# Performance work log

Measured on AMD Instinct MI355X. Metric: run time of the kernel, lower is better.

The kernel has to match this reference:

```python
import jax, jax.numpy as jnp
import numpy as np
from jax.scipy.special import ndtri

D = 1024
BITS = 4
K = 2 ** BITS
N = 4096


def _rotation_matrix(d, seed):
    # Haar-distributed random orthogonal matrix via QR with sign fix,
    # matching generate_rotation_matrix in the torch source.
    g = np.random.default_rng(seed).standard_normal((d, d)).astype(np.float32)
    Q, R = np.linalg.qr(g)
    s = np.sign(np.diag(R))
    s[s == 0] = 1.0
    return jnp.asarray((Q * s[None, :]).astype(np.float32))


def _lloyd_max_centroids(k):
    # Per-coordinate scalar codebook for a standard Gaussian (Lloyd-Max init
    # via inverse-CDF midpoints), analogous to LloydMaxCodebook.centroids [K].
    probs = (jnp.arange(k, dtype=jnp.float32) + 0.5) / k
    return ndtri(probs).astype(jnp.float32)


def setup_inputs() -> dict:
    key = jax.random.key(0)
    x = jax.random.normal(key, (N, D), dtype=jnp.float32)
    Pi = _rotation_matrix(D, seed=42)          # [d, d]
    centroids = _lloyd_max_centroids(K)        # [K]
    return {"x": x, "Pi": Pi, "centroids": centroids}


def reference(x, Pi, centroids):
    # rotate: y = x @ Pi^T
    y = x @ Pi.T                               # [N, d]
    # per-coordinate nearest-centroid argmin over K
    diffs = jnp.abs(y[..., None] - centroids)  # [N, d, K]
    indices = jnp.argmin(diffs, axis=-1)       # [N, d] int
    # dequantize: gather centroids, then unrotate x_hat = y_hat @ Pi
    y_hat = centroids[indices]                 # [N, d]
    x_hat = y_hat @ Pi                         # [N, d]
    return x_hat, indices
```

## Files before the change

### kernel.cpp

```cpp
#include <hip/hip_runtime.h>
#include <hip/hip_bf16.h>

#define TQ_D   1024
#define TQ_KC  16
#define MERGE_K 512
#define TQ_TOL  1.0e-4f
#define LCAP    1024

typedef __attribute__((ext_vector_type(8))) short bf16x8;
typedef __attribute__((ext_vector_type(4))) float f32x4;

__device__ __forceinline__ unsigned short f2bf(float f) {
    union { __hip_bfloat16 h; unsigned short s; } u;
    u.h = __float2bfloat16(f);
    return u.s;
}
__device__ __forceinline__ float bf2f(unsigned short s) {
    union { unsigned int u; float f; } v;
    v.u = (unsigned int)s << 16;
    return v.f;
}

__global__ __launch_bounds__(512)
void tq_rq_mfma(const float* __restrict__ X,
                const float* __restrict__ Pi,
                const float* __restrict__ Cent,
                float* __restrict__ OutIdx,
                unsigned* __restrict__ Counter,
                unsigned* __restrict__ List,
                unsigned cap)
{
    __shared__ unsigned short XhS[128][40];
    __shared__ unsigned short XlS[128][40];
    __shared__ unsigned short PhS[64][40];
    __shared__ unsigned short PlS[64][40];
    __shared__ unsigned lcount;
    __shared__ unsigned gbase;
    __shared__ unsigned llist[LCAP];

    const int tid  = threadIdx.x;
    const int lane = tid & 63;
    const int wv   = tid >> 6;
    const int m0 = blockIdx.y * 128;
    const int n0 = blockIdx.x * 64;
    const int wr = (wv >> 1) * 32;
    const int wc = (wv & 1) * 32;
    const int l15 = lane & 15;
    const int k8  = (lane >> 4) * 8;

    const int srow = tid >> 2;
    const int scol = (tid & 3) * 8;
    const int brow = tid >> 3;
    const int bcol = (tid & 7) * 4;

    const float* aP = X  + (size_t)(m0 + srow) * TQ_D + scol;
    const float* bP = Pi + (size_t)(n0 + brow) * TQ_D + bcol;

    if (tid == 0) lcount = 0;

    f32x4 acc[2][2];
#pragma unroll
    for (int i = 0; i < 2; ++i)
#pragma unroll
        for (int j = 0; j < 2; ++j)
#pragma unroll
            for (int r = 0; r < 4; ++r) acc[i][j][r] = 0.0f;

    float4 va[2], vb;
#pragma unroll
    for (int q = 0; q < 2; ++q) va[q] = *(const float4*)(aP + 4 * q);
    vb = *(const float4*)(bP);

#pragma unroll
    for (int q = 0; q < 2; ++q) {
        ushort4 ah, al;
        const float* fa = (const float*)&va[q];
        ah.x = f2bf(fa[0]); al.x = f2bf(fa[0] - bf2f(ah.x));
        ah.y = f2bf(fa[1]); al.y = f2bf(fa[1] - bf2f(ah.y));
        ah.z = f2bf(fa[2]); al.z = f2bf(fa[2] - bf2f(ah.z));
        ah.w = f2bf(fa[3]); al.w = f2bf(fa[3] - bf2f(ah.w));
        *(ushort4*)&XhS[srow][scol + 4 * q] = ah;
        *(ushort4*)&XlS[srow][scol + 4 * q] = al;
    }
    {
        ushort4 bh, bl;
        const float* fb = (const float*)&vb;
        bh.x = f2bf(fb[0]); bl.x = f2bf(fb[0] - bf2f(bh.x));
        bh.y = f2bf(fb[1]); bl.y = f2bf(fb[1] - bf2f(bh.y));
        bh.z = f2bf(fb[2]); bl.z = f2bf(fb[2] - bf2f(bh.z));
        bh.w = f2bf(fb[3]); bl.w = f2bf(fb[3] - bf2f(bh.w));
        *(ushort4*)&PhS[brow][bcol] = bh;
        *(ushort4*)&PlS[brow][bcol] = bl;
    }
    __syncthreads();

    for (int kt = 0; kt < 32; ++kt) {
        const bool more = (kt + 1) < 32;
        if (more) {
            const float* ap = aP + (kt + 1) * 32;
            const float* bp = bP + (kt + 1) * 32;
#pragma unroll
            for (int q = 0; q < 2; ++q) va[q] = *(const float4*)(ap + 4 * q);
            vb = *(const float4*)(bp);
        }

        bf16x8 afh[2], afl[2], bfh[2], bfl[2];
#pragma unroll
        for (int i = 0; i < 2; ++i) {
            afh[i] = *(const bf16x8*)&XhS[wr + i * 16 + l15][k8];
            afl[i] = *(const bf16x8*)&XlS[wr + i * 16 + l15][k8];
        }
#pragma unroll
        for (int j = 0; j < 2; ++j) {
            bfh[j] = *(const bf16x8*)&PhS[wc + j * 16 + l15][k8];
            bfl[j] = *(const bf16x8*)&PlS[wc + j * 16 + l15][k8];
        }

#pragma unroll
        for (int i = 0; i < 2; ++i)
#pragma unroll
            for (int j = 0; j < 2; ++j) {
                acc[i][j] = __builtin_amdgcn_mfma_f32_16x16x32_bf16(
                    afh[i], bfh[j], acc[i][j], 0, 0, 0);
                acc[i][j] = __builtin_amdgcn_mfma_f32_16x16x32_bf16(
                    afl[i], bfh[j], acc[i][j], 0, 0, 0);
                acc[i][j] = __builtin_amdgcn_mfma_f32_16x16x32_bf16(
                    afh[i], bfl[j], acc[i][j], 0, 0, 0);
                acc[i][j] = __builtin_amdgcn_mfma_f32_16x16x32_bf16(
                    afl[i], bfl[j], acc[i][j], 0, 0, 0);
            }

        if (more) {
            __syncthreads();
#pragma unroll
            for (int q = 0; q < 2; ++q) {
                ushort4 ah, al;
                const float* fa = (const float*)&va[q];
                ah.x = f2bf(fa[0]); al.x = f2bf(fa[0] - bf2f(ah.x));
                ah.y = f2bf(fa[1]); al.y = f2bf(fa[1] - bf2f(ah.y));
                ah.z = f2bf(fa[2]); al.z = f2bf(fa[2] - bf2f(ah.z));
                ah.w = f2bf(fa[3]); al.w = f2bf(fa[3] - bf2f(ah.w));
                *(ushort4*)&XhS[srow][scol + 4 * q] = ah;
                *(ushort4*)&XlS[srow][scol + 4 * q] = al;
            }
            {
                ushort4 bh, bl;
                const float* fb = (const float*)&vb;
                bh.x = f2bf(fb[0]); bl.x = f2bf(fb[0] - bf2f(bh.x));
                bh.y = f2bf(fb[1]); bl.y = f2bf(fb[1] - bf2f(bh.y));
                bh.z = f2bf(fb[2]); bl.z = f2bf(fb[2] - bf2f(bh.z));
                bh.w = f2bf(fb[3]); bl.w = f2bf(fb[3] - bf2f(bh.w));
                *(ushort4*)&PhS[brow][bcol] = bh;
                *(ushort4*)&PlS[brow][bcol] = bl;
            }
            __syncthreads();
        }
    }

    float c[TQ_KC];
#pragma unroll
    for (int q = 0; q < TQ_KC; ++q) c[q] = Cent[q];

#pragma unroll
    for (int i = 0; i < 2; ++i)
#pragma unroll
        for (int j = 0; j < 2; ++j)
#pragma unroll
            for (int r = 0; r < 4; ++r) {
                const int row = m0 + wr + i * 16 + (lane >> 4) * 4 + r;
                const int col = n0 + wc + j * 16 + l15;
                const float y = acc[i][j][r];
                int best = 0;
                float bd = fabsf(y - c[0]);
#pragma unroll
                for (int q = 1; q < TQ_KC; ++q) {
                    const float d = fabsf(y - c[q]);
                    if (d < bd) { bd = d; best = q; }
                }
                float dist = 1e30f;
#pragma unroll
                for (int q = 0; q < TQ_KC - 1; ++q) {
                    const float mid = 0.5f * (c[q] + c[q + 1]);
                    dist = fminf(dist, fabsf(y - mid));
                }
                if (dist < TQ_TOL) {
                    const unsigned id = ((unsigned)row << 10) | (unsigned)col;
                    const unsigned ls = atomicAdd(&lcount, 1u);
                    if (ls < LCAP) {
                        llist[ls] = id;
                    } else {
                        const unsigned gs = atomicAdd(Counter, 1u);
                        if (gs < cap) List[gs] = id;
                    }
                }
                OutIdx[(size_t)row * TQ_D + col] = (float)best;
            }

    __syncthreads();
    if (tid == 0) {
        const unsigned cnt = min(lcount, (unsigned)LCAP);
        gbase = (cnt > 0) ? atomicAdd(Counter, cnt) : 0u;
    }
    __syncthreads();
    const unsigned cnt = min(lcount, (unsigned)LCAP);
    for (unsigned s = tid; s < cnt; s += 512) {
        const unsigned g = gbase + s;
        if (g < cap) List[g] = llist[s];
    }
}

__global__ __launch_bounds__(256)
void tq_fixup_lds(const float* __restrict__ X,
                  const float* __restrict__ Pi,
                  const float* __restrict__ Cent,
                  float* __restrict__ OutIdx,
                  const unsigned* __restrict__ Counter,
                  const unsigned* __restrict__ List,
                  unsigned cap)
{
    __shared__ float Rows[8][2][1024];
    __shared__ float part[8][2];
    __shared__ unsigned ids[8];

    const int tid = threadIdx.x;
    const unsigned count = min(*Counter, cap);

    for (unsigned base = blockIdx.x * 8; base < count; base += gridDim.x * 8) {
        const unsigned nsus = min(8u, count - base);

        if (tid < 8) ids[tid] = (tid < nsus) ? List[base + tid] : 0u;
        __syncthreads();

#pragma unroll
        for (int q = 0; q < 16; ++q) {
            const int lin = q * 256 + tid;
            const int sus = lin >> 9;
            const int rowsel = (lin >> 8) & 1;
            const int f4 = lin & 255;
            if ((unsigned)sus < nsus) {
                const unsigned id = ids[sus];
                const int m = id >> 10;
                const int n = id & (TQ_D - 1);
                const float* src = rowsel ? (Pi + (size_t)n * TQ_D)
                                          : (X + (size_t)m * TQ_D);
                *(float4*)&Rows[sus][rowsel][f4 * 4] =
                    *(const float4*)(src + f4 * 4);
            }
        }
        __syncthreads();

        if (tid < 16 && (unsigned)(tid >> 1) < nsus) {
            const int sus = tid >> 1;
            const int p = tid & 1;
            const int kb = p * MERGE_K;
            float a = 0.0f;
            for (int k = 0; k < MERGE_K; k += 4) {
                const float4 xa = *(const float4*)&Rows[sus][0][kb + k];
                const float4 pa = *(const float4*)&Rows[sus][1][kb + k];
                a = fmaf(xa.x, pa.x, a);
                a = fmaf(xa.y, pa.y, a);
                a = fmaf(xa.z, pa.z, a);
                a = fmaf(xa.w, pa.w, a);
            }
            part[sus][p] = a;
        }
        __syncthreads();

        if (tid < (int)nsus) {
            const float y = part[tid][0] + part[tid][1];
            float c[TQ_KC];
#pragma unroll
            for (int q = 0; q < TQ_KC; ++q) c[q] = Cent[q];
            int best = 0;
            float bd = fabsf(y - c[0]);
#pragma unroll
            for (int q = 1; q < TQ_KC; ++q) {
                const float d = fabsf(y - c[q]);
                if (d < bd) { bd = d; best = q; }
            }
            const unsigned id = ids[tid];
            OutIdx[(size_t)(id >> 10) * TQ_D + (id & (TQ_D - 1))] = (float)best;
        }
        __syncthreads();
    }
}

__global__ __launch_bounds__(512)
void tq_dq_mfma(const float* __restrict__ IdxF,
                const float* __restrict__ Pi,
                const float* __restrict__ Cent,
                float* __restrict__ Xhat)
{
    __shared__ unsigned short Ys[128][40];
    __shared__ unsigned short Ps[64][40];
    __shared__ unsigned short csb[TQ_KC];

    const int tid  = threadIdx.x;
    const int lane = tid & 63;
    const int wv   = tid >> 6;
    const int m0 = blockIdx.y * 128;
    const int n0 = blockIdx.x * 64;
    const int wr = (wv >> 1) * 32;
    const int wc = (wv & 1) * 32;
    const int l15 = lane & 15;
    const int k8  = (lane >> 4) * 8;

    const int srow = tid >> 2;
    const int scol = (tid & 3) * 8;
    const int bk = tid >> 4;
    const int bnq = (tid & 15) * 4;

    const float* aP = IdxF + (size_t)(m0 + srow) * TQ_D + scol;
    const float* bP = Pi + (size_t)bk * TQ_D + n0 + bnq;

    if (tid < TQ_KC) csb[tid] = f2bf(Cent[tid]);

    f32x4 acc[2][2];
#pragma unroll
    for (int i = 0; i < 2; ++i)
#pragma unroll
        for (int j = 0; j < 2; ++j)
#pragma unroll
            for (int r = 0; r < 4; ++r) acc[i][j][r] = 0.0f;

    float4 va[2], vb;
#pragma unroll
    for (int q = 0; q < 2; ++q) va[q] = *(const float4*)(aP + 4 * q);
    vb = *(const float4*)(bP);

    __syncthreads();

#pragma unroll
    for (int q = 0; q < 2; ++q) {
        ushort4 w;
        const float* fa = (const float*)&va[q];
        w.x = csb[(int)fa[0] & 15];
        w.y = csb[(int)fa[1] & 15];
        w.z = csb[(int)fa[2] & 15];
        w.w = csb[(int)fa[3] & 15];
        *(ushort4*)&Ys[srow][scol + 4 * q] = w;
    }
    {
        const float* fb = (const float*)&vb;
        Ps[bnq + 0][bk] = f2bf(fb[0]);
        Ps[bnq + 1][bk] = f2bf(fb[1]);
        Ps[bnq + 2][bk] = f2bf(fb[2]);
        Ps[bnq + 3][bk] = f2bf(fb[3]);
    }
    __syncthreads();

    for (int kt = 0; kt < 32; ++kt) {
        const bool more = (kt + 1) < 32;
        if (more) {
            const float* ap = aP + (kt + 1) * 32;
            const float* bp = bP + (size_t)(kt + 1) * 32 * TQ_D;
#pragma unroll
            for (int q = 0; q < 2; ++q) va[q] = *(const float4*)(ap + 4 * q);
            vb = *(const float4*)(bp);
        }

        bf16x8 af[2], bfr[2];
#pragma unroll
        for (int i = 0; i < 2; ++i)
            af[i] = *(const bf16x8*)&Ys[wr + i * 16 + l15][k8];
#pragma unroll
        for (int j = 0; j < 2; ++j)
            bfr[j] = *(const bf16x8*)&Ps[wc + j * 16 + l15][k8];

#pragma unroll
        for (int i = 0; i < 2; ++i)
#pragma unroll
            for (int j = 0; j < 2; ++j)
                acc[i][j] = __builtin_amdgcn_mfma_f32_16x16x32_bf16(
                    af[i], bfr[j], acc[i][j], 0, 0, 0);

        if (more) {
            __syncthreads();
#pragma unroll
            for (int q = 0; q < 2; ++q) {
                ushort4 w;
                const float* fa = (const float*)&va[q];
                w.x = csb[(int)fa[0] & 15];
                w.y = csb[(int)fa[1] & 15];
                w.z = csb[(int)fa[2] & 15];
                w.w = csb[(int)fa[3] & 15];
                *(ushort4*)&Ys[srow][scol + 4 * q] = w;
            }
            {
                const float* fb = (const float*)&vb;
                Ps[bnq + 0][bk] = f2bf(fb[0]);
                Ps[bnq + 1][bk] = f2bf(fb[1]);
                Ps[bnq + 2][bk] = f2bf(fb[2]);
                Ps[bnq + 3][bk] = f2bf(fb[3]);
            }
            __syncthreads();
        }
    }

#pragma unroll
    for (int i = 0; i < 2; ++i)
#pragma unroll
        for (int j = 0; j < 2; ++j)
#pragma unroll
            for (int r = 0; r < 4; ++r) {
                const int row = wr + i * 16 + (lane >> 4) * 4 + r;
                const int col = wc + j * 16 + l15;
                Xhat[(size_t)(m0 + row) * TQ_D + n0 + col] = acc[i][j][r];
            }
}

extern "C" void kernel_launch(void* const* d_in, const int* in_sizes, int n_in,
                              void* d_out, int out_size, void* d_ws, size_t ws_size,
                              hipStream_t stream)
{
    const float* x    = (const float*)d_in[0];
    const float* Pi   = (const float*)d_in[1];
    const float* cent = (const float*)d_in[2];
    float* out = (float*)d_out;

    const int ND = in_sizes[0];
    const int N  = ND / TQ_D;

    float* xhat = out;
    float* oidx = out + ND;

    unsigned* counter = (unsigned*)xhat;
    unsigned* list    = (unsigned*)xhat + 16;
    const unsigned cap = (unsigned)(ND - 16);

    hipMemsetAsync(counter, 0, 4, stream);

    dim3 grid1(TQ_D / 64, N / 128);
    tq_rq_mfma<<<grid1, 512, 0, stream>>>(x, Pi, cent, oidx, counter, list, cap);

    tq_fixup_lds<<<1024, 256, 0, stream>>>(x, Pi, cent, oidx, counter, list, cap);

    tq_dq_mfma<<<grid1, 512, 0, stream>>>(oidx, Pi, cent, xhat);
}
```

Baseline: 107.4 us.

## Pre-split inputs into bf16 hi/lo buffers and dequantize from bf16 centroids

```diff
diff --git a/kernel.cpp b/kernel.cpp
--- a/kernel.cpp
+++ b/kernel.cpp
@@ -8,6 +8,7 @@
 #define LCAP    1024
 
 typedef __attribute__((ext_vector_type(8))) short bf16x8;
+typedef __attribute__((ext_vector_type(8))) unsigned short ushort8;
 typedef __attribute__((ext_vector_type(4))) float f32x4;
 
 __device__ __forceinline__ unsigned short f2bf(float f) {
@@ -19,6 +20,188 @@
     union { unsigned int u; float f; } v;
     v.u = (unsigned int)s << 16;
     return v.f;
+}
+
+__global__ __launch_bounds__(256)
+void tq_split(const float* __restrict__ In,
+              unsigned short* __restrict__ Hi,
+              unsigned short* __restrict__ Lo,
+              int total4)
+{
+    for (int i = blockIdx.x * 256 + threadIdx.x; i < total4;
+         i += gridDim.x * 256) {
+        const float4 v = *((const float4*)In + i);
+        ushort4 h, l;
+        h.x = f2bf(v.x); l.x = f2bf(v.x - bf2f(h.x));
+        h.y = f2bf(v.y); l.y = f2bf(v.y - bf2f(h.y));
+        h.z = f2bf(v.z); l.z = f2bf(v.z - bf2f(h.z));
+        h.w = f2bf(v.w); l.w = f2bf(v.w - bf2f(h.w));
+        *((ushort4*)Hi + i) = h;
+        *((ushort4*)Lo + i) = l;
+    }
+}
+
+__global__ __launch_bounds__(512)
+void tq_rq_mfma_pre(const unsigned short* __restrict__ Xh,
+                    const unsigned short* __restrict__ Xl,
+                    const unsigned short* __restrict__ Ph,
+                    const unsigned short* __restrict__ Pl,
+                    const float* __restrict__ Cent,
+                    float* __restrict__ OutIdx,
+                    unsigned short* __restrict__ Yh,
+                    unsigned* __restrict__ Counter,
+                    unsigned* __restrict__ List,
+                    unsigned cap)
+{
+    __shared__ unsigned short XhS[128][40];
+    __shared__ unsigned short XlS[128][40];
+    __shared__ unsigned short PhS[64][40];
+    __shared__ unsigned short PlS[64][40];
+    __shared__ unsigned lcount;
+    __shared__ unsigned gbase;
+    __shared__ unsigned llist[LCAP];
+
+    const int tid  = threadIdx.x;
+    const int lane = tid & 63;
+    const int wv   = tid >> 6;
+    const int m0 = blockIdx.y * 128;
+    const int n0 = blockIdx.x * 64;
+    const int wr = (wv >> 1) * 32;
+    const int wc = (wv & 1) * 32;
+    const int l15 = lane & 15;
+    const int k8  = (lane >> 4) * 8;
+
+    const int srow = tid >> 2;
+    const int scol = (tid & 3) * 8;
+    const int brow = tid >> 3;
+    const int bcol = (tid & 7) * 4;
+
+    const unsigned short* aH = Xh + (size_t)(m0 + srow) * TQ_D + scol;
+    const unsigned short* aL = Xl + (size_t)(m0 + srow) * TQ_D + scol;
+    const unsigned short* bH = Ph + (size_t)(n0 + brow) * TQ_D + bcol;
+    const unsigned short* bL = Pl + (size_t)(n0 + brow) * TQ_D + bcol;
+
+    if (tid == 0) lcount = 0;
+
+    f32x4 acc[2][2];
+#pragma unroll
+    for (int i = 0; i < 2; ++i)
+#pragma unroll
+        for (int j = 0; j < 2; ++j)
+#pragma unroll
+            for (int r = 0; r < 4; ++r) acc[i][j][r] = 0.0f;
+
+    ushort8 vah, val;
+    ushort4 vbh, vbl;
+    vah = *(const ushort8*)(aH);
+    val = *(const ushort8*)(aL);
+    vbh = *(const ushort4*)(bH);
+    vbl = *(const ushort4*)(bL);
+
+    *(ushort8*)&XhS[srow][scol] = vah;
+    *(ushort8*)&XlS[srow][scol] = val;
+    *(ushort4*)&PhS[brow][bcol] = vbh;
+    *(ushort4*)&PlS[brow][bcol] = vbl;
+    __syncthreads();
+
+    for (int kt = 0; kt < 32; ++kt) {
+        const bool more = (kt + 1) < 32;
+        if (more) {
+            const int off = (kt + 1) * 32;
+            vah = *(const ushort8*)(aH + off);
+            val = *(const ushort8*)(aL + off);
+            vbh = *(const ushort4*)(bH + off);
+            vbl = *(const ushort4*)(bL + off);
+        }
+
+        bf16x8 afh[2], afl[2], bfh[2], bfl[2];
+#pragma unroll
+        for (int i = 0; i < 2; ++i) {
+            afh[i] = *(const bf16x8*)&XhS[wr + i * 16 + l15][k8];
+            afl[i] = *(const bf16x8*)&XlS[wr + i * 16 + l15][k8];
+        }
+#pragma unroll
+        for (int j = 0; j < 2; ++j) {
+            bfh[j] = *(const bf16x8*)&PhS[wc + j * 16 + l15][k8];
+            bfl[j] = *(const bf16x8*)&PlS[wc + j * 16 + l15][k8];
+        }
+
+#pragma unroll
+        for (int i = 0; i < 2; ++i)
+#pragma unroll
+            for (int j = 0; j < 2; ++j) {
+                acc[i][j] = __builtin_amdgcn_mfma_f32_16x16x32_bf16(
+                    afh[i], bfh[j], acc[i][j], 0, 0, 0);
+                acc[i][j] = __builtin_amdgcn_mfma_f32_16x16x32_bf16(
+                    afl[i], bfh[j], acc[i][j], 0, 0, 0);
+                acc[i][j] = __builtin_amdgcn_mfma_f32_16x16x32_bf16(
+                    afh[i], bfl[j], acc[i][j], 0, 0, 0);
+                acc[i][j] = __builtin_amdgcn_mfma_f32_16x16x32_bf16(
+                    afl[i], bfl[j], acc[i][j], 0, 0, 0);
+            }
+
+        if (more) {
+            __syncthreads();
+            *(ushort8*)&XhS[srow][scol] = vah;
+            *(ushort8*)&XlS[srow][scol] = val;
+            *(ushort4*)&PhS[brow][bcol] = vbh;
+            *(ushort4*)&PlS[brow][bcol] = vbl;
+            __syncthreads();
+        }
+    }
+
+    float c[TQ_KC];
+#pragma unroll
+    for (int q = 0; q < TQ_KC; ++q) c[q] = Cent[q];
+
+#pragma unroll
+    for (int i = 0; i < 2; ++i)
+#pragma unroll
+        for (int j = 0; j < 2; ++j)
+#pragma unroll
+            for (int r = 0; r < 4; ++r) {
+                const int row = m0 + wr + i * 16 + (lane >> 4) * 4 + r;
+                const int col = n0 + wc + j * 16 + l15;
+                const float y = acc[i][j][r];
+                int best = 0;
+                float bd = fabsf(y - c[0]);
+#pragma unroll
+                for (int q = 1; q < TQ_KC; ++q) {
+                    const float d = fabsf(y - c[q]);
+                    if (d < bd) { bd = d; best = q; }
+                }
+                float dist = 1e30f;
+#pragma unroll
+                for (int q = 0; q < TQ_KC - 1; ++q) {
+                    const float mid = 0.5f * (c[q] + c[q + 1]);
+                    dist = fminf(dist, fabsf(y - mid));
+                }
+                if (dist < TQ_TOL) {
+                    const unsigned id = ((unsigned)row << 10) | (unsigned)col;
+                    const unsigned ls = atomicAdd(&lcount, 1u);
+                    if (ls < LCAP) {
+                        llist[ls] = id;
+                    } else {
+                        const unsigned gs = atomicAdd(Counter, 1u);
+                        if (gs < cap) List[gs] = id;
+                    }
+                }
+                const size_t e = (size_t)row * TQ_D + col;
+                OutIdx[e] = (float)best;
+                Yh[e] = f2bf(c[best]);
+            }
+
+    __syncthreads();
+    if (tid == 0) {
+        const unsigned cnt = min(lcount, (unsigned)LCAP);
+        gbase = (cnt > 0) ? atomicAdd(Counter, cnt) : 0u;
+    }
+    __syncthreads();
+    const unsigned cnt = min(lcount, (unsigned)LCAP);
+    for (unsigned s = tid; s < cnt; s += 512) {
+        const unsigned g = gbase + s;
+        if (g < cap) List[g] = llist[s];
+    }
 }
 
 __global__ __launch_bounds__(512)
@@ -214,6 +397,7 @@
                   const float* __restrict__ Pi,
                   const float* __restrict__ Cent,
                   float* __restrict__ OutIdx,
+                  unsigned short* __restrict__ Yh,
                   const unsigned* __restrict__ Counter,
                   const unsigned* __restrict__ List,
                   unsigned cap)
@@ -279,10 +463,101 @@
                 if (d < bd) { bd = d; best = q; }
             }
             const unsigned id = ids[tid];
-            OutIdx[(size_t)(id >> 10) * TQ_D + (id & (TQ_D - 1))] = (float)best;
+            const size_t e = (size_t)(id >> 10) * TQ_D + (id & (TQ_D - 1));
+            OutIdx[e] = (float)best;
+            if (Yh) Yh[e] = f2bf(c[best]);
         }
         __syncthreads();
     }
+}
+
+__global__ __launch_bounds__(512)
+void tq_dq_mfma_pre(const unsigned short* __restrict__ Yh,
+                    const unsigned short* __restrict__ Ph,
+                    float* __restrict__ Xhat)
+{
+    __shared__ unsigned short Ys[128][40];
+    __shared__ unsigned short Ps[64][40];
+
+    const int tid  = threadIdx.x;
+    const int lane = tid & 63;
+    const int wv   = tid >> 6;
+    const int m0 = blockIdx.y * 128;
+    const int n0 = blockIdx.x * 64;
+    const int wr = (wv >> 1) * 32;
+    const int wc = (wv & 1) * 32;
+    const int l15 = lane & 15;
+    const int k8  = (lane >> 4) * 8;
+
+    const int srow = tid >> 2;
+    const int scol = (tid & 3) * 8;
+    const int bk = tid >> 4;
+    const int bnq = (tid & 15) * 4;
+
+    const unsigned short* aP = Yh + (size_t)(m0 + srow) * TQ_D + scol;
+    const unsigned short* bP = Ph + (size_t)bk * TQ_D + n0 + bnq;
+
+    f32x4 acc[2][2];
+#pragma unroll
+    for (int i = 0; i < 2; ++i)
+#pragma unroll
+        for (int j = 0; j < 2; ++j)
+#pragma unroll
+            for (int r = 0; r < 4; ++r) acc[i][j][r] = 0.0f;
+
+    ushort8 va = *(const ushort8*)(aP);
+    ushort4 vb = *(const ushort4*)(bP);
+
+    *(ushort8*)&Ys[srow][scol] = va;
+    Ps[bnq + 0][bk] = vb.x;
+    Ps[bnq + 1][bk] = vb.y;
+    Ps[bnq + 2][bk] = vb.z;
+    Ps[bnq + 3][bk] = vb.w;
+    __syncthreads();
+
+    for (int kt = 0; kt < 32; ++kt) {
+        const bool more = (kt + 1) < 32;
+        if (more) {
+            va = *(const ushort8*)(aP + (kt + 1) * 32);
+            vb = *(const ushort4*)(bP + (size_t)(kt + 1) * 32 * TQ_D);
+        }
+
+        bf16x8 af[2], bfr[2];
+#pragma unroll
+        for (int i = 0; i < 2; ++i)
+            af[i] = *(const bf16x8*)&Ys[wr + i * 16 + l15][k8];
+#pragma unroll
+        for (int j = 0; j < 2; ++j)
+            bfr[j] = *(const bf16x8*)&Ps[wc + j * 16 + l15][k8];
+
+#pragma unroll
+        for (int i = 0; i < 2; ++i)
+#pragma unroll
+            for (int j = 0; j < 2; ++j)
+                acc[i][j] = __builtin_amdgcn_mfma_f32_16x16x32_bf16(
+                    af[i], bfr[j], acc[i][j], 0, 0, 0);
+
+        if (more) {
+            __syncthreads();
+            *(ushort8*)&Ys[srow][scol] = va;
+            Ps[bnq + 0][bk] = vb.x;
+            Ps[bnq + 1][bk] = vb.y;
+            Ps[bnq + 2][bk] = vb.z;
+            Ps[bnq + 3][bk] = vb.w;
+            __syncthreads();
+        }
+    }
+
+#pragma unroll
+    for (int i = 0; i < 2; ++i)
+#pragma unroll
+        for (int j = 0; j < 2; ++j)
+#pragma unroll
+            for (int r = 0; r < 4; ++r) {
+                const int row = wr + i * 16 + (lane >> 4) * 4 + r;
+                const int col = wc + j * 16 + l15;
+                Xhat[(size_t)(m0 + row) * TQ_D + n0 + col] = acc[i][j][r];
+            }
 }
 
 __global__ __launch_bounds__(512)
@@ -419,6 +694,7 @@
     float* out = (float*)d_out;
 
     const int ND = in_sizes[0];
+    const int DD = in_sizes[1];
     const int N  = ND / TQ_D;
 
     float* xhat = out;
@@ -431,9 +707,27 @@
     hipMemsetAsync(counter, 0, 4, stream);
 
     dim3 grid1(TQ_D / 64, N / 128);
-    tq_rq_mfma<<<grid1, 512, 0, stream>>>(x, Pi, cent, oidx, counter, list, cap);
-
-    tq_fixup_lds<<<1024, 256, 0, stream>>>(x, Pi, cent, oidx, counter, list, cap);
-
-    tq_dq_mfma<<<grid1, 512, 0, stream>>>(oidx, Pi, cent, xhat);
-}
+
+    const size_t wsNeed = 2ull * (3ull * ND + 2ull * DD);
+    if (ws_size >= wsNeed) {
+        unsigned short* Xh = (unsigned short*)d_ws;
+        unsigned short* Xl = Xh + ND;
+        unsigned short* Ph = Xl + ND;
+        unsigned short* Pl = Ph + DD;
+        unsigned short* Yh = Pl + DD;
+
+        tq_split<<<2048, 256, 0, stream>>>(x, Xh, Xl, ND / 4);
+        tq_split<<<1024, 256, 0, stream>>>(Pi, Ph, Pl, DD / 4);
+        tq_rq_mfma_pre<<<grid1, 512, 0, stream>>>(Xh, Xl, Ph, Pl, cent, oidx,
+                                                  Yh, counter, list, cap);
+        tq_fixup_lds<<<1024, 256, 0, stream>>>(x, Pi, cent, oidx, Yh,
+                                               counter, list, cap);
+        tq_dq_mfma_pre<<<grid1, 512, 0, stream>>>(Yh, Ph, xhat);
+    } else {
+        tq_rq_mfma<<<grid1, 512, 0, stream>>>(x, Pi, cent, oidx,
+                                              counter, list, cap);
+        tq_fixup_lds<<<1024, 256, 0, stream>>>(x, Pi, cent, oidx, nullptr,
+                                               counter, list, cap);
+        tq_dq_mfma<<<grid1, 512, 0, stream>>>(oidx, Pi, cent, xhat);
+    }
+}
```

After: 112.4 us. 4.6% more time.
